# Kernel optimization log

Measured on AMD Instinct MI355X. Metric: run time of the kernel, lower is better.

The kernel has to match this reference:

```python
import jax, jax.numpy as jnp
import numpy as np

B, S, V, E, H, NL, NM = 32, 4096, 256, 128, 256, 3, 16


def setup_inputs() -> dict:
    key = jax.random.key(0)
    ks = jax.random.split(key, 8)
    return {
        "x": jax.random.randint(ks[0], (B, S), 0, V),
        "emb": jax.random.normal(ks[1], (V, E), jnp.float32) * 0.02,
        "W0": jax.random.normal(ks[2], (2 * H, E), jnp.float32) / np.sqrt(E).astype(np.float32),
        "b0": jnp.zeros((2 * H,), jnp.float32),
        "Wl": jax.random.normal(ks[3], (NL - 1, 2 * H, H), jnp.float32) / np.sqrt(H).astype(np.float32),
        "bl": jnp.zeros((NL - 1, 2 * H), jnp.float32),
        "Walign": jax.random.normal(ks[4], (H, E), jnp.float32) / np.sqrt(E).astype(np.float32),
        "Wout": jax.random.normal(ks[5], (V, H), jnp.float32) / np.sqrt(H).astype(np.float32),
        "bout": jnp.zeros((V,), jnp.float32),
        "num_memorize": NM,
    }


def _log_g(x):
    # log of g(x) = x + 0.5 for x >= 0, sigmoid(x) otherwise
    return jnp.where(x >= 0, jnp.log(jax.nn.relu(x) + 0.5), -jax.nn.softplus(-x))


def _mingru_scan(gate, hid):
    # Heinsen log-space parallel scan of h_t = (1-z_t) h_{t-1} + z_t g(hid_t),
    # z_t = sigmoid(gate_t), h_0 = g(0) = 0.5.  gate/hid: [B,S,H]
    log_z = -jax.nn.softplus(-gate)          # log sigmoid(gate)
    log_coeffs = -jax.nn.softplus(gate)      # log(1 - z)
    log_h0 = jnp.full(gate[:, :1].shape, jnp.log(0.5).astype(gate.dtype), gate.dtype)
    a_star = jnp.cumsum(jnp.pad(log_coeffs, ((0, 0), (1, 0), (0, 0))), axis=1)  # [B,S+1,H]
    log_vals = jnp.concatenate([log_h0, log_z + _log_g(hid)], axis=1)           # [B,S+1,H]
    h = jnp.exp(a_star + jax.lax.cumlogsumexp(log_vals - a_star, axis=1))
    return h[:, 1:]  # [B,S,H]


def reference(x, emb, W0, b0, Wl, bl, Walign, Wout, bout, num_memorize):
    h_in = emb[x]  # [B,S,E]
    # layer 0 (input dims E -> H, residual via alignment projection)
    gh = jnp.einsum('bse,ge->bsg', h_in, W0) + b0
    gate, hid = jnp.split(gh, 2, axis=-1)
    h = _mingru_scan(gate, hid) + jnp.einsum('bse,he->bsh', h_in, Walign)
    # layers 1..NL-1 (H -> H, identity residual)
    for i in range(Wl.shape[0]):
        gh = jnp.einsum('bsh,gh->bsg', h, Wl[i]) + bl[i]
        gate, hid = jnp.split(gh, 2, axis=-1)
        h = _mingru_scan(gate, hid) + h
    logits = jnp.einsum('bsh,vh->bsv', h, Wout) + bout  # [B,S,V]
    return logits[:, -num_memorize:]
```

## Files before the change

### kernel.cpp

```cpp
#include <hip/hip_runtime.h>
#include <hip/hip_bf16.h>

using bf16 = __hip_bfloat16;

constexpr int B_ = 32, S_ = 4096, V_ = 256, E_ = 128, H_ = 256, NM_ = 16;
constexpr int GH = 2 * H_;
constexpr int NC = 128, L_ = 32;

typedef __attribute__((ext_vector_type(8))) short bf16x8;
typedef __attribute__((ext_vector_type(4))) float f32x4;

__device__ __forceinline__ float b2f(unsigned short u) {
  union { float f; unsigned int i; } x; x.i = ((unsigned int)u) << 16; return x.f;
}
__device__ __forceinline__ unsigned short f2b(float f) {
  unsigned int i = __builtin_bit_cast(unsigned int, f);
  return (unsigned short)((i + 0x7fffu + ((i >> 16) & 1u)) >> 16);
}
__device__ __forceinline__ float hi_f(unsigned int u) {
  union { float f; unsigned int i; } x; x.i = u & 0xffff0000u; return x.f;
}
__device__ __forceinline__ float lo_f(unsigned int u) {
  union { float f; unsigned int i; } x; x.i = u << 16; return x.f;
}
__device__ __forceinline__ unsigned int cvt_pk(float lb, float ha) {
  unsigned int r;
  asm("v_cvt_pk_bf16_f32 %0, %1, %2" : "=v"(r) : "v"(lb), "v"(ha));
  return r;
}

__device__ __forceinline__ void step_ab(float gate, float hid, float& a, float& bt) {
  const float LOG2E = 1.4426950408889634f;
  float e  = __builtin_amdgcn_exp2f(gate * LOG2E);
  a = __builtin_amdgcn_rcpf(1.0f + e);
  float sn = __builtin_amdgcn_rcpf(1.0f + __builtin_amdgcn_exp2f(-hid * LOG2E));
  float g  = (hid >= 0.0f) ? (hid + 0.5f) : sn;
  bt = (1.0f - a) * g;
}

#define ATS(row, bcol) (((row) << 9) | ((bcol) ^ (((row) & 7) << 4)))


__global__ __launch_bounds__(256) void build_tables(
    const float* __restrict__ emb, const float* __restrict__ W0,
    const float* __restrict__ b0, const float* __restrict__ Walign,
    const float* __restrict__ Wl, float* __restrict__ T0, bf16* __restrict__ Wpk) {
  const int v = blockIdx.x;
  const int t = threadIdx.x;
  __shared__ float e[E_];
  if (t < E_) e[t] = emb[v * E_ + t];
  __syncthreads();
  const float4* w0g = (const float4*)(W0 + (size_t)t * E_);
  const float4* w0h = (const float4*)(W0 + (size_t)(t + 256) * E_);
  const float4* wal = (const float4*)(Walign + (size_t)t * E_);
  float g = b0[t], hd = b0[t + 256], al = 0.0f;
  #pragma unroll 8
  for (int k = 0; k < E_ / 4; ++k) {
    float4 ev = *(const float4*)(e + 4 * k);
    float4 ga = w0g[k]; g  += ga.x * ev.x + ga.y * ev.y + ga.z * ev.z + ga.w * ev.w;
    float4 hb = w0h[k]; hd += hb.x * ev.x + hb.y * ev.y + hb.z * ev.z + hb.w * ev.w;
    float4 aw = wal[k]; al += aw.x * ev.x + aw.y * ev.y + aw.z * ev.z + aw.w * ev.w;
  }
  float a, btv; step_ab(g, hd, a, btv);
  T0[(size_t)v * 768 + t]       = a;
  T0[(size_t)v * 768 + 256 + t] = btv;
  T0[(size_t)v * 768 + 512 + t] = al;

  const int fid = v * 256 + t;
  if (fid < 32768) {
    const int layer = fid >> 14;
    const int kk   = (fid >> 11) & 7;
    const int grp  = (fid >> 6) & 31;
    const int lane = fid & 63;
    const int row = grp * 16 + (lane & 15);
    const int k0  = kk * 32 + (lane >> 4) * 8;
    const float* src = Wl + (((size_t)layer * 512 + row) * 256 + k0);
    bf16* dst = Wpk + (size_t)fid * 8;
    #pragma unroll
    for (int e2 = 0; e2 < 8; ++e2) dst[e2] = __float2bfloat16(src[e2]);
  }
}

__global__ __launch_bounds__(256) void scanA_l0(const int* __restrict__ x, const float* __restrict__ T0,
                                                float* __restrict__ cAB) {
  const int b = blockIdx.y;
  const int wv = threadIdx.x >> 6, lane = threadIdx.x & 63;
  const int c = blockIdx.x * 4 + wv;
  const int t4 = lane * 4;
  const int* xp = x + (size_t)b * S_ + (size_t)c * L_;
  float A0=1,A1=1,A2=1,A3=1, B0=0,B1=0,B2=0,B3=0;
  #pragma unroll 4
  for (int t = 0; t < L_; ++t) {
    const float* tp = T0 + (size_t)xp[t] * 768;
    float4 a4 = *(const float4*)(tp + t4);
    float4 b4 = *(const float4*)(tp + 256 + t4);
    A0 = a4.x*A0; B0 = a4.x*B0 + b4.x;
    A1 = a4.y*A1; B1 = a4.y*B1 + b4.y;
    A2 = a4.z*A2; B2 = a4.z*B2 + b4.z;
    A3 = a4.w*A3; B3 = a4.w*B3 + b4.w;
  }
  float* o = cAB + (size_t)(b * NC + c) * 2 * H_;
  *(float4*)(o + t4)      = make_float4(A0, A1, A2, A3);
  *(float4*)(o + H_ + t4) = make_float4(B0, B1, B2, B3);
}

__global__ __launch_bounds__(256) void scanB(const float* __restrict__ cAB, float* __restrict__ cHin) {
  const int b = blockIdx.x, ch = threadIdx.x;
  const float* base = cAB + (size_t)b * NC * 2 * H_ + ch;
  float* out = cHin + (size_t)b * NC * H_ + ch;
  float a[8], bb[8], an[8], bn[8];
  #pragma unroll
  for (int i = 0; i < 8; ++i) { a[i] = base[(size_t)i * 2 * H_]; bb[i] = base[(size_t)i * 2 * H_ + H_]; }
  float hp = 0.5f;
  for (int tile = 0; tile < NC / 8; ++tile) {
    if (tile < NC / 8 - 1) {
      const float* nb = base + (size_t)(tile + 1) * 8 * 2 * H_;
      #pragma unroll
      for (int i = 0; i < 8; ++i) { an[i] = nb[(size_t)i * 2 * H_]; bn[i] = nb[(size_t)i * 2 * H_ + H_]; }
    }
    #pragma unroll
    for (int i = 0; i < 8; ++i) {
      out[(size_t)(tile * 8 + i) * H_] = hp;
      hp = a[i] * hp + bb[i];
    }
    #pragma unroll
    for (int i = 0; i < 8; ++i) { a[i] = an[i]; bb[i] = bn[i]; }
  }
}

__device__ __forceinline__ void gemm_tile(const char* smem, const bf16* __restrict__ Wp,
                                          int lane, int wave,
                                          f32x4 (&accG)[2][4], f32x4 (&accH)[2][4]) {
  const int l15 = lane & 15, lhi = lane >> 4;
  #pragma unroll
  for (int kk = 0; kk < 8; ++kk) {
    const int kb = kk * 64 + lhi * 16;
    bf16x8 af[2], bG[4], bH[4];
    #pragma unroll
    for (int ni = 0; ni < 4; ++ni) {
      bG[ni] = *(const bf16x8*)(Wp + ((size_t)(kk * 2048 + (wave * 4 + ni) * 64 + lane)) * 8);
      bH[ni] = *(const bf16x8*)(Wp + ((size_t)(kk * 2048 + (16 + wave * 4 + ni) * 64 + lane)) * 8);
    }
    #pragma unroll
    for (int mi = 0; mi < 2; ++mi) {
      const int r = mi * 16 + l15;
      af[mi] = *(const bf16x8*)(smem + ATS(r, kb));
    }
    #pragma unroll
    for (int mi = 0; mi < 2; ++mi)
      #pragma unroll
      for (int ni = 0; ni < 4; ++ni) {
        accG[mi][ni] = __builtin_amdgcn_mfma_f32_16x16x32_bf16(af[mi], bG[ni], accG[mi][ni], 0, 0, 0);
        accH[mi][ni] = __builtin_amdgcn_mfma_f32_16x16x32_bf16(af[mi], bH[ni], accH[mi][ni], 0, 0, 0);
      }
  }
}

__device__ __forceinline__ void epilogue_fold(
    const f32x4 (&accG)[2][4], const f32x4 (&accH)[2][4],
    const float* __restrict__ bias, int lane, int wave,
    const char* __restrict__ smemA,
    const float* __restrict__ hm1s,
    unsigned int* __restrict__ scr,
    uint4* __restrict__ ghc4, bool doStore,
    float* __restrict__ o) {
  const int l15 = lane & 15, lhi = lane >> 4;
  #pragma unroll
  for (int ni = 0; ni < 4; ++ni) {
    const int colG = wave * 64 + ni * 16 + l15;
    const float bg = bias[colG], bh = bias[colG + 256];
    float segA[2], segB[2];
    #pragma unroll
    for (int mi = 0; mi < 2; ++mi) {
      const int r0 = mi * 16 + lhi * 4;
      float hprev = (r0 == 0) ? hm1s[colG]
                  : b2f(*(const unsigned short*)(smemA + ATS(r0 - 1, colG * 2)));
      float Aa = 1.0f, Bb = 0.0f;
      unsigned int pk[4];
      #pragma unroll
      for (int j = 0; j < 4; ++j) {
        float a, btv;
        step_ab(accG[mi][ni][j] + bg, accH[mi][ni][j] + bh, a, btv);
        float hcurr = b2f(*(const unsigned short*)(smemA + ATS(r0 + j, colG * 2)));
        float bp = btv + hcurr - a * hprev;
        hprev = hcurr;
        pk[j] = cvt_pk(bp, a);
        const float ar = hi_f(pk[j]), br = lo_f(pk[j]);
        Aa = ar * Aa; Bb = ar * Bb + br;
      }
      if (doStore) {
        unsigned int* wp = scr + l15 * 32 + (((mi * 16 + lhi * 4)) ^ ((l15 & 7) << 2));
        *(uint4*)wp = make_uint4(pk[0], pk[1], pk[2], pk[3]);
      }
      segA[mi] = Aa; segB[mi] = Bb;
    }
    if (doStore) {
      #pragma unroll
      for (int s = 0; s < 2; ++s) {
        const int lin = s * 64 + lane;
        const int ch = lin >> 3, uq = lin & 7;
        uint4 v = *(const uint4*)(scr + ch * 32 + ((uq * 4) ^ ((ch & 7) << 2)));
        ghc4[(size_t)(wave * 64 + ni * 16) * 8 + lin] = v;
      }
    }
    #pragma unroll
    for (int mi = 0; mi < 2; ++mi) {
      float A = segA[mi], Bv = segB[mi];
      {
        float Ap = __shfl_xor(A, 16), Bp = __shfl_xor(Bv, 16);
        float Bn = (lhi & 1) ? (A * Bp + Bv) : (Ap * Bv + Bp);
        A = A * Ap; Bv = Bn;
      }
      {
        float Ap = __shfl_xor(A, 32), Bp = __shfl_xor(Bv, 32);
        float Bn = (lhi & 2) ? (A * Bp + Bv) : (Ap * Bv + Bp);
        A = A * Ap; Bv = Bn;
      }
      segA[mi] = A; segB[mi] = Bv;
    }
    const float Ac = segA[1] * segA[0];
    const float Bc = segA[1] * segB[0] + segB[1];
    if (lhi == 0) { o[colG] = Ac; o[H_ + colG] = Bc; }
  }
}

__global__ __launch_bounds__(256, 4) void l0_gemm_scanA(
    const int* __restrict__ x, const float* __restrict__ T0,
    const float* __restrict__ cHin0,
    const bf16* __restrict__ Wp, const float* __restrict__ bias,
    unsigned int* __restrict__ gh2, float* __restrict__ cAB) {
  __shared__ __align__(16) char smem[16384];
  __shared__ unsigned int scrs[4][512];
  __shared__ float hm1s[256];
  __shared__ int xs[32];
  const int bid = blockIdx.x;
  const int c = bid & (NC - 1), b = bid >> 7;
  const size_t row0 = (size_t)b * S_ + (size_t)c * L_;
  const int tid = threadIdx.x, lane = tid & 63, wave = tid >> 6;
  const int ch = tid;

  if (tid < 32) xs[tid] = x[row0 + tid];
  float state = cHin0[((size_t)b * NC + c) * H_ + ch];
  {
    float hm1 = 0.0f;
    if (c > 0) {
      const int xm1 = x[row0 - 1];
      hm1 = b2f(f2b(state + T0[(size_t)xm1 * 768 + 512 + ch]));
    }
    hm1s[ch] = hm1;
  }
  __syncthreads();
  #pragma unroll 8
  for (int t = 0; t < L_; ++t) {
    const float* tp = T0 + (size_t)xs[t] * 768;
    float a = tp[ch], bt = tp[256 + ch], r = tp[512 + ch];
    state = a * state + bt;
    *(unsigned short*)(smem + ATS(t, ch * 2)) = f2b(state + r);
  }
  __syncthreads();

  f32x4 accG[2][4] = {}, accH[2][4] = {};
  gemm_tile(smem, Wp, lane, wave, accG, accH);
  uint4* ghc4 = (uint4*)(gh2 + ((size_t)b * NC + c) * (L_ * 256));
  epilogue_fold(accG, accH, bias, lane, wave, smem, hm1s, scrs[wave], ghc4, true,
                cAB + ((size_t)b * NC + c) * 2 * H_);
}

__global__ __launch_bounds__(256, 4) void scan_gemm(
    unsigned int* __restrict__ gh2, const float* __restrict__ cHin,
    const bf16* __restrict__ Wp, const float* __restrict__ bias,
    float* __restrict__ cAB) {
  __shared__ __align__(16) char smem[16384];
  __shared__ unsigned int scrs[4][512];
  __shared__ float hm1s[256];
  const int bid = blockIdx.x;
  const int c = bid & (NC - 1), b = bid >> 7;
  const int tid = threadIdx.x, lane = tid & 63, wave = tid >> 6;
  const int ch = tid;

  float hp = cHin[((size_t)b * NC + c) * H_ + ch];
  hm1s[ch] = hp;
  const uint4* pq = (const uint4*)(gh2 + ((size_t)b * NC + c) * (L_ * 256)) + ch * 8;
  #pragma unroll
  for (int tt = 0; tt < 8; ++tt) {
    uint4 v = pq[tt];
    hp = hi_f(v.x) * hp + lo_f(v.x);
    *(unsigned short*)(smem + ATS(tt * 4 + 0, ch * 2)) = f2b(hp);
    hp = hi_f(v.y) * hp + lo_f(v.y);
    *(unsigned short*)(smem + ATS(tt * 4 + 1, ch * 2)) = f2b(hp);
    hp = hi_f(v.z) * hp + lo_f(v.z);
    *(unsigned short*)(smem + ATS(tt * 4 + 2, ch * 2)) = f2b(hp);
    hp = hi_f(v.w) * hp + lo_f(v.w);
    *(unsigned short*)(smem + ATS(tt * 4 + 3, ch * 2)) = f2b(hp);
  }
  __syncthreads();

  f32x4 accG[2][4] = {}, accH[2][4] = {};
  gemm_tile(smem, Wp, lane, wave, accG, accH);
  uint4* ghc4 = (uint4*)(gh2 + ((size_t)b * NC + c) * (L_ * 256));
  epilogue_fold(accG, accH, bias, lane, wave, smem, hm1s, scrs[wave], ghc4, c >= NC - 1,
                cAB + ((size_t)b * NC + c) * 2 * H_);
}

__global__ __launch_bounds__(256) void scanC_tail(const unsigned int* __restrict__ gh2,
                                                  const float* __restrict__ cHin,
                                                  bf16* __restrict__ h) {
  const int b = blockIdx.x;
  const int c = NC - 1;
  const int ch = threadIdx.x;
  const size_t row0 = (size_t)b * S_ + (size_t)c * L_;
  float hp = cHin[((size_t)b * NC + c) * H_ + ch];
  const uint4* pq = (const uint4*)(gh2 + ((size_t)b * NC + c) * (L_ * 256)) + ch * 8;
  unsigned short* hio = (unsigned short*)h + row0 * 256 + ch;
  #pragma unroll
  for (int tt = 0; tt < 8; ++tt) {
    uint4 v = pq[tt];
    hp = hi_f(v.x) * hp + lo_f(v.x); hio[(tt * 4 + 0) * 256] = f2b(hp);
    hp = hi_f(v.y) * hp + lo_f(v.y); hio[(tt * 4 + 1) * 256] = f2b(hp);
    hp = hi_f(v.z) * hp + lo_f(v.z); hio[(tt * 4 + 2) * 256] = f2b(hp);
    hp = hi_f(v.w) * hp + lo_f(v.w); hio[(tt * 4 + 3) * 256] = f2b(hp);
  }
}

__global__ __launch_bounds__(256) void out_logits(const bf16* __restrict__ h,
                                                  const float* __restrict__ Wout,
                                                  const float* __restrict__ bout,
                                                  float* __restrict__ out) {
  const int r = blockIdx.x;
  const int b = r >> 4, si = r & 15;
  const int v = threadIdx.x;
  __shared__ float hs[H_];
  const size_t t = (size_t)b * S_ + (S_ - NM_ + si);
  hs[v] = b2f(((const unsigned short*)h)[t * H_ + v]);
  __syncthreads();
  float acc = bout[v];
  const float4* w4 = (const float4*)(Wout + (size_t)v * H_);
  #pragma unroll 8
  for (int k = 0; k < H_ / 4; ++k) {
    float4 wv = w4[k];
    float4 hv = *(const float4*)(hs + 4 * k);
    acc += wv.x * hv.x + wv.y * hv.y + wv.z * hv.z + wv.w * hv.w;
  }
  out[(size_t)r * V_ + v] = acc;
}

extern "C" void kernel_launch(void* const* d_in, const int* in_sizes, int n_in,
                              void* d_out, int out_size, void* d_ws, size_t ws_size,
                              hipStream_t stream) {
  const int*   x      = (const int*)d_in[0];
  const float* emb    = (const float*)d_in[1];
  const float* W0     = (const float*)d_in[2];
  const float* b0     = (const float*)d_in[3];
  const float* Wl     = (const float*)d_in[4];
  const float* bl     = (const float*)d_in[5];
  const float* Walign = (const float*)d_in[6];
  const float* Wout   = (const float*)d_in[7];
  const float* bout   = (const float*)d_in[8];
  (void)in_sizes; (void)n_in; (void)out_size; (void)ws_size;

  char* ws = (char*)d_ws;
  size_t off = 0;
  unsigned int* gh2 = (unsigned int*)(ws + off); off += (size_t)B_ * S_ * 256 * 4;
  bf16*  h    = (bf16*)(ws + off);  off += (size_t)B_ * S_ * H_ * 2;
  float* cAB  = (float*)(ws + off); off += (size_t)B_ * NC * 2 * H_ * 4;
  float* cHin = (float*)(ws + off); off += (size_t)B_ * NC * H_ * 4;
  float* T0   = (float*)(ws + off); off += (size_t)V_ * 768 * 4;
  bf16*  Wpk  = (bf16*)(ws + off);  off += (size_t)2 * GH * H_ * 2;

  build_tables<<<256, 256, 0, stream>>>(emb, W0, b0, Walign, Wl, T0, Wpk);

  dim3 gscan(NC / 4, B_);
  scanA_l0<<<gscan, 256, 0, stream>>>(x, T0, cAB);
  scanB<<<B_, 256, 0, stream>>>(cAB, cHin);

  const bf16* Wpk2 = Wpk + (size_t)GH * H_;
  l0_gemm_scanA<<<B_ * NC, 256, 0, stream>>>(x, T0, cHin, Wpk, bl, gh2, cAB);
  scanB<<<B_, 256, 0, stream>>>(cAB, cHin);
  scan_gemm<<<B_ * NC, 256, 0, stream>>>(gh2, cHin, Wpk2, bl + GH, cAB);
  scanB<<<B_, 256, 0, stream>>>(cAB, cHin);
  scanC_tail<<<B_, 256, 0, stream>>>(gh2, cHin, h);

  out_logits<<<B_ * NM_, 256, 0, stream>>>(h, Wout, bout, (float*)d_out);
}
```

Measured before the change: 203.9 us.

## Process two chunks per block, overlapping second GEMM with first epilogue

Each block of the fused GEMM+scan kernels now handles two adjacent sequence chunks, with half the grid. The prefix scan for both chunks is interleaved, and the second chunk's MFMA k-steps are interleaved with the first chunk's per-column epilogue, so weight-fragment loads are shared in time and latency is hidden. hm1 is now passed by cross-lane shuffle instead of shared memory. It costs more LDS and registers (launch bounds drop to 3 blocks/SM) and halves the number of blocks.

```diff
diff --git a/kernel.cpp b/kernel.cpp
--- a/kernel.cpp
+++ b/kernel.cpp
@@ -128,178 +128,220 @@
   }
 }
 
-__device__ __forceinline__ void gemm_tile(const char* smem, const bf16* __restrict__ Wp,
-                                          int lane, int wave,
-                                          f32x4 (&accG)[2][4], f32x4 (&accH)[2][4]) {
+__device__ __forceinline__ void gemm_kk(const char* tile, const bf16* __restrict__ Wp,
+                                        int kk, int lane, int wave,
+                                        f32x4 (&accG)[2][4], f32x4 (&accH)[2][4]) {
   const int l15 = lane & 15, lhi = lane >> 4;
-  #pragma unroll
-  for (int kk = 0; kk < 8; ++kk) {
-    const int kb = kk * 64 + lhi * 16;
-    bf16x8 af[2], bG[4], bH[4];
+  const int kb = kk * 64 + lhi * 16;
+  bf16x8 af[2], bG[4], bH[4];
+  #pragma unroll
+  for (int ni = 0; ni < 4; ++ni) {
+    bG[ni] = *(const bf16x8*)(Wp + ((size_t)(kk * 2048 + (wave * 4 + ni) * 64 + lane)) * 8);
+    bH[ni] = *(const bf16x8*)(Wp + ((size_t)(kk * 2048 + (16 + wave * 4 + ni) * 64 + lane)) * 8);
+  }
+  #pragma unroll
+  for (int mi = 0; mi < 2; ++mi)
+    af[mi] = *(const bf16x8*)(tile + ATS(mi * 16 + l15, kb));
+  #pragma unroll
+  for (int mi = 0; mi < 2; ++mi)
     #pragma unroll
     for (int ni = 0; ni < 4; ++ni) {
-      bG[ni] = *(const bf16x8*)(Wp + ((size_t)(kk * 2048 + (wave * 4 + ni) * 64 + lane)) * 8);
-      bH[ni] = *(const bf16x8*)(Wp + ((size_t)(kk * 2048 + (16 + wave * 4 + ni) * 64 + lane)) * 8);
-    }
-    #pragma unroll
-    for (int mi = 0; mi < 2; ++mi) {
-      const int r = mi * 16 + l15;
-      af[mi] = *(const bf16x8*)(smem + ATS(r, kb));
-    }
-    #pragma unroll
-    for (int mi = 0; mi < 2; ++mi)
-      #pragma unroll
-      for (int ni = 0; ni < 4; ++ni) {
-        accG[mi][ni] = __builtin_amdgcn_mfma_f32_16x16x32_bf16(af[mi], bG[ni], accG[mi][ni], 0, 0, 0);
-        accH[mi][ni] = __builtin_amdgcn_mfma_f32_16x16x32_bf16(af[mi], bH[ni], accH[mi][ni], 0, 0, 0);
-      }
-  }
-}
-
-__device__ __forceinline__ void epilogue_fold(
-    const f32x4 (&accG)[2][4], const f32x4 (&accH)[2][4],
+      accG[mi][ni] = __builtin_amdgcn_mfma_f32_16x16x32_bf16(af[mi], bG[ni], accG[mi][ni], 0, 0, 0);
+      accH[mi][ni] = __builtin_amdgcn_mfma_f32_16x16x32_bf16(af[mi], bH[ni], accH[mi][ni], 0, 0, 0);
+    }
+}
+
+__device__ __forceinline__ void epilogue_ni(
+    int ni, const f32x4 (&accG)[2][4], const f32x4 (&accH)[2][4],
     const float* __restrict__ bias, int lane, int wave,
-    const char* __restrict__ smemA,
-    const float* __restrict__ hm1s,
-    unsigned int* __restrict__ scr,
-    uint4* __restrict__ ghc4, bool doStore,
+    const char* __restrict__ smemA, float hm1,
+    unsigned int* __restrict__ scr, uint4* __restrict__ ghc4, bool doStore,
     float* __restrict__ o) {
   const int l15 = lane & 15, lhi = lane >> 4;
-  #pragma unroll
-  for (int ni = 0; ni < 4; ++ni) {
-    const int colG = wave * 64 + ni * 16 + l15;
-    const float bg = bias[colG], bh = bias[colG + 256];
-    float segA[2], segB[2];
-    #pragma unroll
-    for (int mi = 0; mi < 2; ++mi) {
-      const int r0 = mi * 16 + lhi * 4;
-      float hprev = (r0 == 0) ? hm1s[colG]
-                  : b2f(*(const unsigned short*)(smemA + ATS(r0 - 1, colG * 2)));
-      float Aa = 1.0f, Bb = 0.0f;
-      unsigned int pk[4];
-      #pragma unroll
-      for (int j = 0; j < 4; ++j) {
-        float a, btv;
-        step_ab(accG[mi][ni][j] + bg, accH[mi][ni][j] + bh, a, btv);
-        float hcurr = b2f(*(const unsigned short*)(smemA + ATS(r0 + j, colG * 2)));
-        float bp = btv + hcurr - a * hprev;
-        hprev = hcurr;
-        pk[j] = cvt_pk(bp, a);
-        const float ar = hi_f(pk[j]), br = lo_f(pk[j]);
-        Aa = ar * Aa; Bb = ar * Bb + br;
-      }
-      if (doStore) {
-        unsigned int* wp = scr + l15 * 32 + (((mi * 16 + lhi * 4)) ^ ((l15 & 7) << 2));
-        *(uint4*)wp = make_uint4(pk[0], pk[1], pk[2], pk[3]);
-      }
-      segA[mi] = Aa; segB[mi] = Bb;
+  const int colG = wave * 64 + ni * 16 + l15;
+  const float bg = bias[colG], bh = bias[colG + 256];
+  float segA[2], segB[2];
+  #pragma unroll
+  for (int mi = 0; mi < 2; ++mi) {
+    const int r0 = mi * 16 + lhi * 4;
+    float hprev = (r0 == 0) ? hm1
+                : b2f(*(const unsigned short*)(smemA + ATS(r0 - 1, colG * 2)));
+    float Aa = 1.0f, Bb = 0.0f;
+    unsigned int pk[4];
+    #pragma unroll
+    for (int j = 0; j < 4; ++j) {
+      float a, btv;
+      step_ab(accG[mi][ni][j] + bg, accH[mi][ni][j] + bh, a, btv);
+      float hcurr = b2f(*(const unsigned short*)(smemA + ATS(r0 + j, colG * 2)));
+      float bp = btv + hcurr - a * hprev;
+      hprev = hcurr;
+      pk[j] = cvt_pk(bp, a);
+      const float ar = hi_f(pk[j]), br = lo_f(pk[j]);
+      Aa = ar * Aa; Bb = ar * Bb + br;
     }
     if (doStore) {
-      #pragma unroll
-      for (int s = 0; s < 2; ++s) {
-        const int lin = s * 64 + lane;
-        const int ch = lin >> 3, uq = lin & 7;
-        uint4 v = *(const uint4*)(scr + ch * 32 + ((uq * 4) ^ ((ch & 7) << 2)));
-        ghc4[(size_t)(wave * 64 + ni * 16) * 8 + lin] = v;
-      }
-    }
-    #pragma unroll
-    for (int mi = 0; mi < 2; ++mi) {
-      float A = segA[mi], Bv = segB[mi];
-      {
-        float Ap = __shfl_xor(A, 16), Bp = __shfl_xor(Bv, 16);
-        float Bn = (lhi & 1) ? (A * Bp + Bv) : (Ap * Bv + Bp);
-        A = A * Ap; Bv = Bn;
-      }
-      {
-        float Ap = __shfl_xor(A, 32), Bp = __shfl_xor(Bv, 32);
-        float Bn = (lhi & 2) ? (A * Bp + Bv) : (Ap * Bv + Bp);
-        A = A * Ap; Bv = Bn;
-      }
-      segA[mi] = A; segB[mi] = Bv;
-    }
-    const float Ac = segA[1] * segA[0];
-    const float Bc = segA[1] * segB[0] + segB[1];
-    if (lhi == 0) { o[colG] = Ac; o[H_ + colG] = Bc; }
-  }
-}
-
-__global__ __launch_bounds__(256, 4) void l0_gemm_scanA(
+      unsigned int* wp = scr + l15 * 32 + (((mi * 16 + lhi * 4)) ^ ((l15 & 7) << 2));
+      *(uint4*)wp = make_uint4(pk[0], pk[1], pk[2], pk[3]);
+    }
+    segA[mi] = Aa; segB[mi] = Bb;
+  }
+  if (doStore) {
+    #pragma unroll
+    for (int s = 0; s < 2; ++s) {
+      const int lin = s * 64 + lane;
+      const int ch = lin >> 3, uq = lin & 7;
+      uint4 v = *(const uint4*)(scr + ch * 32 + ((uq * 4) ^ ((ch & 7) << 2)));
+      ghc4[(size_t)(wave * 64 + ni * 16) * 8 + lin] = v;
+    }
+  }
+  #pragma unroll
+  for (int mi = 0; mi < 2; ++mi) {
+    float A = segA[mi], Bv = segB[mi];
+    {
+      float Ap = __shfl_xor(A, 16), Bp = __shfl_xor(Bv, 16);
+      float Bn = (lhi & 1) ? (A * Bp + Bv) : (Ap * Bv + Bp);
+      A = A * Ap; Bv = Bn;
+    }
+    {
+      float Ap = __shfl_xor(A, 32), Bp = __shfl_xor(Bv, 32);
+      float Bn = (lhi & 2) ? (A * Bp + Bv) : (Ap * Bv + Bp);
+      A = A * Ap; Bv = Bn;
+    }
+    segA[mi] = A; segB[mi] = Bv;
+  }
+  const float Ac = segA[1] * segA[0];
+  const float Bc = segA[1] * segB[0] + segB[1];
+  if (lhi == 0) { o[colG] = Ac; o[H_ + colG] = Bc; }
+}
+
+__global__ __launch_bounds__(256, 3) void l0_gemm_scanA(
     const int* __restrict__ x, const float* __restrict__ T0,
     const float* __restrict__ cHin0,
     const bf16* __restrict__ Wp, const float* __restrict__ bias,
     unsigned int* __restrict__ gh2, float* __restrict__ cAB) {
-  __shared__ __align__(16) char smem[16384];
-  __shared__ unsigned int scrs[4][512];
-  __shared__ float hm1s[256];
-  __shared__ int xs[32];
+  __shared__ __align__(16) char smem[40960];
+  __shared__ int xs[64];
+  char* tileA = smem;
+  char* tileB = smem + 16384;
   const int bid = blockIdx.x;
-  const int c = bid & (NC - 1), b = bid >> 7;
-  const size_t row0 = (size_t)b * S_ + (size_t)c * L_;
+  const int cp = bid & 63, b = bid >> 6;
+  const int c0 = cp * 2, c1 = c0 + 1;
+  const size_t row0 = (size_t)b * S_ + (size_t)c0 * L_;
+  const size_t row1 = row0 + L_;
   const int tid = threadIdx.x, lane = tid & 63, wave = tid >> 6;
   const int ch = tid;
-
-  if (tid < 32) xs[tid] = x[row0 + tid];
-  float state = cHin0[((size_t)b * NC + c) * H_ + ch];
-  {
-    float hm1 = 0.0f;
-    if (c > 0) {
-      const int xm1 = x[row0 - 1];
-      hm1 = b2f(f2b(state + T0[(size_t)xm1 * 768 + 512 + ch]));
-    }
-    hm1s[ch] = hm1;
-  }
+  unsigned int* scr = (unsigned int*)(smem + 32768) + wave * 512;
+
+  if (tid < 64) xs[tid] = x[row0 + tid];
+  float st0 = cHin0[((size_t)b * NC + c0) * H_ + ch];
+  float st1 = cHin0[((size_t)b * NC + c1) * H_ + ch];
+  float hm1_0 = 0.0f;
+  if (c0 > 0) hm1_0 = b2f(f2b(st0 + T0[(size_t)x[row0 - 1] * 768 + 512 + ch]));
+  float hm1_1 = b2f(f2b(st1 + T0[(size_t)x[row1 - 1] * 768 + 512 + ch]));
   __syncthreads();
-  #pragma unroll 8
+  #pragma unroll 4
   for (int t = 0; t < L_; ++t) {
-    const float* tp = T0 + (size_t)xs[t] * 768;
-    float a = tp[ch], bt = tp[256 + ch], r = tp[512 + ch];
-    state = a * state + bt;
-    *(unsigned short*)(smem + ATS(t, ch * 2)) = f2b(state + r);
+    const float* tp0 = T0 + (size_t)xs[t] * 768;
+    const float* tp1 = T0 + (size_t)xs[32 + t] * 768;
+    float a0 = tp0[ch], bt0 = tp0[256 + ch], r0 = tp0[512 + ch];
+    float a1 = tp1[ch], bt1 = tp1[256 + ch], r1 = tp1[512 + ch];
+    st0 = a0 * st0 + bt0;
+    st1 = a1 * st1 + bt1;
+    *(unsigned short*)(tileA + ATS(t, ch * 2)) = f2b(st0 + r0);
+    *(unsigned short*)(tileB + ATS(t, ch * 2)) = f2b(st1 + r1);
   }
   __syncthreads();
 
-  f32x4 accG[2][4] = {}, accH[2][4] = {};
-  gemm_tile(smem, Wp, lane, wave, accG, accH);
-  uint4* ghc4 = (uint4*)(gh2 + ((size_t)b * NC + c) * (L_ * 256));
-  epilogue_fold(accG, accH, bias, lane, wave, smem, hm1s, scrs[wave], ghc4, true,
-                cAB + ((size_t)b * NC + c) * 2 * H_);
-}
-
-__global__ __launch_bounds__(256, 4) void scan_gemm(
+  const int l15 = lane & 15;
+  f32x4 aG[2][4] = {}, aH[2][4] = {};
+  #pragma unroll
+  for (int kk = 0; kk < 8; ++kk) gemm_kk(tileA, Wp, kk, lane, wave, aG, aH);
+
+  uint4* g4_0 = (uint4*)(gh2 + ((size_t)b * NC + c0) * (L_ * 256));
+  uint4* g4_1 = (uint4*)(gh2 + ((size_t)b * NC + c1) * (L_ * 256));
+  float* o0 = cAB + ((size_t)b * NC + c0) * 2 * H_;
+  float* o1 = cAB + ((size_t)b * NC + c1) * 2 * H_;
+
+  f32x4 bG2[2][4] = {}, bH2[2][4] = {};
+  #pragma unroll
+  for (int grp = 0; grp < 4; ++grp) {
+    gemm_kk(tileB, Wp, 2 * grp,     lane, wave, bG2, bH2);
+    gemm_kk(tileB, Wp, 2 * grp + 1, lane, wave, bG2, bH2);
+    float hm1 = __shfl(hm1_0, grp * 16 + l15);
+    epilogue_ni(grp, aG, aH, bias, lane, wave, tileA, hm1, scr, g4_0, true, o0);
+  }
+  #pragma unroll
+  for (int grp = 0; grp < 4; ++grp) {
+    float hm1 = __shfl(hm1_1, grp * 16 + l15);
+    epilogue_ni(grp, bG2, bH2, bias, lane, wave, tileB, hm1, scr, g4_1, true, o1);
+  }
+}
+
+__global__ __launch_bounds__(256, 3) void scan_gemm(
     unsigned int* __restrict__ gh2, const float* __restrict__ cHin,
     const bf16* __restrict__ Wp, const float* __restrict__ bias,
     float* __restrict__ cAB) {
-  __shared__ __align__(16) char smem[16384];
-  __shared__ unsigned int scrs[4][512];
-  __shared__ float hm1s[256];
+  __shared__ __align__(16) char smem[40960];
+  char* tileA = smem;
+  char* tileB = smem + 16384;
   const int bid = blockIdx.x;
-  const int c = bid & (NC - 1), b = bid >> 7;
+  const int cp = bid & 63, b = bid >> 6;
+  const int c0 = cp * 2, c1 = c0 + 1;
   const int tid = threadIdx.x, lane = tid & 63, wave = tid >> 6;
   const int ch = tid;
-
-  float hp = cHin[((size_t)b * NC + c) * H_ + ch];
-  hm1s[ch] = hp;
-  const uint4* pq = (const uint4*)(gh2 + ((size_t)b * NC + c) * (L_ * 256)) + ch * 8;
+  unsigned int* scr = (unsigned int*)(smem + 32768) + wave * 512;
+
+  float hp0 = cHin[((size_t)b * NC + c0) * H_ + ch];
+  float hp1 = cHin[((size_t)b * NC + c1) * H_ + ch];
+  const float hp0i = hp0, hp1i = hp1;
+  const uint4* pq0 = (const uint4*)(gh2 + ((size_t)b * NC + c0) * (L_ * 256)) + ch * 8;
+  const uint4* pq1 = (const uint4*)(gh2 + ((size_t)b * NC + c1) * (L_ * 256)) + ch * 8;
   #pragma unroll
   for (int tt = 0; tt < 8; ++tt) {
-    uint4 v = pq[tt];
-    hp = hi_f(v.x) * hp + lo_f(v.x);
-    *(unsigned short*)(smem + ATS(tt * 4 + 0, ch * 2)) = f2b(hp);
-    hp = hi_f(v.y) * hp + lo_f(v.y);
-    *(unsigned short*)(smem + ATS(tt * 4 + 1, ch * 2)) = f2b(hp);
-    hp = hi_f(v.z) * hp + lo_f(v.z);
-    *(unsigned short*)(smem + ATS(tt * 4 + 2, ch * 2)) = f2b(hp);
-    hp = hi_f(v.w) * hp + lo_f(v.w);
-    *(unsigned short*)(smem + ATS(tt * 4 + 3, ch * 2)) = f2b(hp);
+    uint4 v0 = pq0[tt], v1 = pq1[tt];
+    hp0 = hi_f(v0.x) * hp0 + lo_f(v0.x);
+    hp1 = hi_f(v1.x) * hp1 + lo_f(v1.x);
+    *(unsigned short*)(tileA + ATS(tt * 4 + 0, ch * 2)) = f2b(hp0);
+    *(unsigned short*)(tileB + ATS(tt * 4 + 0, ch * 2)) = f2b(hp1);
+    hp0 = hi_f(v0.y) * hp0 + lo_f(v0.y);
+    hp1 = hi_f(v1.y) * hp1 + lo_f(v1.y);
+    *(unsigned short*)(tileA + ATS(tt * 4 + 1, ch * 2)) = f2b(hp0);
+    *(unsigned short*)(tileB + ATS(tt * 4 + 1, ch * 2)) = f2b(hp1);
+    hp0 = hi_f(v0.z) * hp0 + lo_f(v0.z);
+    hp1 = hi_f(v1.z) * hp1 + lo_f(v1.z);
+    *(unsigned short*)(tileA + ATS(tt * 4 + 2, ch * 2)) = f2b(hp0);
+    *(unsigned short*)(tileB + ATS(tt * 4 + 2, ch * 2)) = f2b(hp1);
+    hp0 = hi_f(v0.w) * hp0 + lo_f(v0.w);
+    hp1 = hi_f(v1.w) * hp1 + lo_f(v1.w);
+    *(unsigned short*)(tileA + ATS(tt * 4 + 3, ch * 2)) = f2b(hp0);
+    *(unsigned short*)(tileB + ATS(tt * 4 + 3, ch * 2)) = f2b(hp1);
   }
   __syncthreads();
 
-  f32x4 accG[2][4] = {}, accH[2][4] = {};
-  gemm_tile(smem, Wp, lane, wave, accG, accH);
-  uint4* ghc4 = (uint4*)(gh2 + ((size_t)b * NC + c) * (L_ * 256));
-  epilogue_fold(accG, accH, bias, lane, wave, smem, hm1s, scrs[wave], ghc4, c >= NC - 1,
-                cAB + ((size_t)b * NC + c) * 2 * H_);
+  const int l15 = lane & 15;
+  f32x4 aG[2][4] = {}, aH[2][4] = {};
+  #pragma unroll
+  for (int kk = 0; kk < 8; ++kk) gemm_kk(tileA, Wp, kk, lane, wave, aG, aH);
+
+  uint4* g4_0 = (uint4*)(gh2 + ((size_t)b * NC + c0) * (L_ * 256));
+  uint4* g4_1 = (uint4*)(gh2 + ((size_t)b * NC + c1) * (L_ * 256));
+  float* o0 = cAB + ((size_t)b * NC + c0) * 2 * H_;
+  float* o1 = cAB + ((size_t)b * NC + c1) * 2 * H_;
+  const bool st1 = (c1 == NC - 1);
+
+  f32x4 bG2[2][4] = {}, bH2[2][4] = {};
+  #pragma unroll
+  for (int grp = 0; grp < 4; ++grp) {
+    gemm_kk(tileB, Wp, 2 * grp,     lane, wave, bG2, bH2);
+    gemm_kk(tileB, Wp, 2 * grp + 1, lane, wave, bG2, bH2);
+    float hm1 = __shfl(hp0i, grp * 16 + l15);
+    epilogue_ni(grp, aG, aH, bias, lane, wave, tileA, hm1, scr, g4_0, false, o0);
+  }
+  #pragma unroll
+  for (int grp = 0; grp < 4; ++grp) {
+    float hm1 = __shfl(hp1i, grp * 16 + l15);
+    epilogue_ni(grp, bG2, bH2, bias, lane, wave, tileB, hm1, scr, g4_1, st1, o1);
+  }
 }
 
 __global__ __launch_bounds__(256) void scanC_tail(const unsigned int* __restrict__ gh2,
@@ -374,9 +416,9 @@
   scanB<<<B_, 256, 0, stream>>>(cAB, cHin);
 
   const bf16* Wpk2 = Wpk + (size_t)GH * H_;
-  l0_gemm_scanA<<<B_ * NC, 256, 0, stream>>>(x, T0, cHin, Wpk, bl, gh2, cAB);
+  l0_gemm_scanA<<<B_ * NC / 2, 256, 0, stream>>>(x, T0, cHin, Wpk, bl, gh2, cAB);
   scanB<<<B_, 256, 0, stream>>>(cAB, cHin);
-  scan_gemm<<<B_ * NC, 256, 0, stream>>>(gh2, cHin, Wpk2, bl + GH, cAB);
+  scan_gemm<<<B_ * NC / 2, 256, 0, stream>>>(gh2, cHin, Wpk2, bl + GH, cAB);
   scanB<<<B_, 256, 0, stream>>>(cAB, cHin);
   scanC_tail<<<B_, 256, 0, stream>>>(gh2, cHin, h);
 
```

After: 612.3 us. 3x slower.
